# Kernel optimization log

Measured on AMD Instinct MI355X. Metric: run time of the kernel, lower is better.

The kernel has to match this reference:

```python
import jax, jax.numpy as jnp
import numpy as np

B, S = 10000, 32        # batch nodes, sampled neighbors per node
N, D_IN, D_H = 100000, 512, 512


def setup_inputs() -> dict:
    key = jax.random.key(0)
    k1, k2, k3 = jax.random.split(key, 3)
    neigh_idx = jax.random.randint(k1, (B, S), 0, N)                 # int neighbor ids
    features = jax.random.normal(k2, (N, D_IN), dtype=jnp.float32)   # node feature table
    W = jax.random.normal(k3, (D_H, D_IN), dtype=jnp.float32) * (1.0 / np.sqrt(D_IN))
    b = jnp.zeros((D_H,), dtype=jnp.float32)
    return {"neigh_idx": neigh_idx, "features": features, "W": W, "b": b}


def reference(neigh_idx, features, W, b):
    # gather neighbor embeddings: [B, S, D_IN]
    neigh_feats = features[neigh_idx]
    # MLP: Linear(input_dim, hidden_dim) + ReLU  -> [B, S, D_H]
    h = jax.nn.relu(jnp.einsum("bsd,hd->bsh", neigh_feats, W) + b)
    # mask-based mean pool over sampled neighbors (mask @ embed / row_sum) -> [B, D_H]
    return jnp.mean(h, axis=1)
```

## Files before the change

### kernel.cpp

```cpp
#include <hip/hip_runtime.h>
#include <hip/hip_bf16.h>


#define S_NB 32
#define D_IN 512
#define D_H  512
#define BM   128
#define BN   128
#define BK   64
#define NNODE 100000
#define NBATCH 10000
#define NTILE_N 4
#define NTILE_M 784
#define NTILES  (NTILE_N * NTILE_M)

typedef __attribute__((ext_vector_type(8))) short  short8;
typedef __attribute__((ext_vector_type(4))) float  f32x4;
typedef __attribute__((ext_vector_type(4))) unsigned short us4;
typedef __attribute__((ext_vector_type(8))) unsigned short us8;

__device__ __forceinline__ unsigned short f2bf(float x) {
  union { float f; unsigned u; } v; v.f = x;
  unsigned r = v.u + 0x7FFFu + ((v.u >> 16) & 1u);
  return (unsigned short)(r >> 16);
}

__device__ __forceinline__ float bf2f(unsigned short x) {
  union { unsigned u; float f; } v; v.u = ((unsigned)x) << 16;
  return v.f;
}

__device__ __forceinline__ int swz(int row, int cb) {
  return row * 128 + (cb ^ ((row & 7) << 4));
}

__device__ __forceinline__ void gld_lds16(const unsigned short* g, unsigned short* l) {
  __builtin_amdgcn_global_load_lds(
      (const __attribute__((address_space(1))) unsigned int*)g,
      (__attribute__((address_space(3))) unsigned int*)l, 16, 0, 0);
}

__global__ __launch_bounds__(256, 8)
void cvt_bf16(const float* __restrict__ src, unsigned short* __restrict__ dst, int n8) {
  int i = blockIdx.x * blockDim.x + threadIdx.x;
  const int stride = gridDim.x * blockDim.x;
  for (; i < n8; i += stride) {
    f32x4 a = *(const f32x4*)(src + (size_t)i * 8);
    f32x4 b = *(const f32x4*)(src + (size_t)i * 8 + 4);
    us8 o;
    o[0] = f2bf(a.x); o[1] = f2bf(a.y); o[2] = f2bf(a.z); o[3] = f2bf(a.w);
    o[4] = f2bf(b.x); o[5] = f2bf(b.y); o[6] = f2bf(b.z); o[7] = f2bf(b.w);
    *(us8*)(dst + (size_t)i * 8) = o;
  }
}

__global__ __launch_bounds__(256, 3)
void gemm_hf2(const float* __restrict__ feat,
              const unsigned short* __restrict__ Wb,
              const float* __restrict__ bias,
              unsigned short* __restrict__ Hb) {
  const int tid  = threadIdx.x;
  const int lane = tid & 63;
  const int wid  = tid >> 6;
  const int wr   = wid >> 1;
  const int wc   = wid & 1;

  const int bid  = blockIdx.x;
  const int tile = (bid & 7) * (NTILES / 8) + (bid >> 3);
  const int n0   = (tile & 3) * BN;
  const int m0   = (tile >> 2) * BM;

  __shared__ __align__(16) unsigned short As[BM * BK];
  __shared__ __align__(16) unsigned short Bs[2][BM * BK];

  const int lr = tid >> 4;
  const int lc = tid & 15;
  const float* aptr[8];
  int awoff[8];
#pragma unroll
  for (int p = 0; p < 8; ++p) {
    int row = p * 16 + lr;
    int gr  = m0 + row; if (gr > NNODE - 1) gr = NNODE - 1;
    aptr[p]  = feat + (size_t)gr * D_IN + lc * 4;
    awoff[p] = swz(row, lc * 8);
  }

  const unsigned short* srcW[4];
  int wdoff[4];
#pragma unroll
  for (int i = 0; i < 4; ++i) {
    int rl = wid * 32 + i * 8 + (lane >> 3);
    int g  = (lane & 7) ^ (rl & 7);
    srcW[i]  = Wb + (size_t)(n0 + rl) * D_IN + g * 8;
    wdoff[i] = (wid * 32 + i * 8) * 64;
  }

  f32x4 acc[4][4];
#pragma unroll
  for (int i = 0; i < 4; ++i)
#pragma unroll
    for (int j = 0; j < 4; ++j)
      acc[i][j] = (f32x4){0.f, 0.f, 0.f, 0.f};

  const int frow = lane & 15;
  const int kcb  = (lane >> 4) * 16;
  const int arow = wr * 64 + frow;
  const int brow = wc * 64 + frow;

  {
    f32x4 a0[8];
#pragma unroll
    for (int p = 0; p < 8; ++p) a0[p] = *(const f32x4*)(aptr[p]);
#pragma unroll
    for (int i = 0; i < 4; ++i) gld_lds16(srcW[i], &Bs[0][wdoff[i]]);
#pragma unroll
    for (int p = 0; p < 8; ++p) {
      us4 v;
      v.x = f2bf(a0[p].x); v.y = f2bf(a0[p].y); v.z = f2bf(a0[p].z); v.w = f2bf(a0[p].w);
      *(us4*)((char*)As + awoff[p]) = v;
    }
  }
  __syncthreads();

#pragma unroll
  for (int ki = 0; ki < D_IN / BK; ++ki) {
    const int cur = ki & 1;

    f32x4 an[8];
    if (ki < D_IN / BK - 1) {
#pragma unroll
      for (int p = 0; p < 8; ++p) an[p] = *(const f32x4*)(aptr[p] + (ki + 1) * BK);
#pragma unroll
      for (int i = 0; i < 4; ++i) gld_lds16(srcW[i] + (ki + 1) * BK, &Bs[cur ^ 1][wdoff[i]]);
    }

#pragma unroll
    for (int kk = 0; kk < 2; ++kk) {
      short8 af[4], bfr[4];
#pragma unroll
      for (int mi = 0; mi < 4; ++mi)
        af[mi] = *(const short8*)((const char*)As + swz(arow + mi * 16, kk * 64 + kcb));
#pragma unroll
      for (int ni = 0; ni < 4; ++ni)
        bfr[ni] = *(const short8*)((const char*)Bs[cur] + swz(brow + ni * 16, kk * 64 + kcb));
#pragma unroll
      for (int mi = 0; mi < 4; ++mi)
#pragma unroll
        for (int ni = 0; ni < 4; ++ni)
          acc[mi][ni] = __builtin_amdgcn_mfma_f32_16x16x32_bf16(af[mi], bfr[ni], acc[mi][ni], 0, 0, 0);
    }

    __syncthreads();

    if (ki < D_IN / BK - 1) {
#pragma unroll
      for (int p = 0; p < 8; ++p) {
        us4 v;
        v.x = f2bf(an[p].x); v.y = f2bf(an[p].y); v.z = f2bf(an[p].z); v.w = f2bf(an[p].w);
        *(us4*)((char*)As + awoff[p]) = v;
      }
    }
    __syncthreads();
  }

  unsigned short* Cs = &Bs[0][0];
  const int rq = lane >> 4;
#pragma unroll
  for (int ni = 0; ni < 4; ++ni) {
    int col = wc * 64 + ni * 16 + frow;
    float bv = bias[n0 + col];
#pragma unroll
    for (int mi = 0; mi < 4; ++mi) {
#pragma unroll
      for (int r = 0; r < 4; ++r) {
        int row = wr * 64 + mi * 16 + rq * 4 + r;
        int byt = row * 256 + ((col * 2) ^ ((row & 7) << 4));
        *(unsigned short*)((char*)Cs + byt) = f2bf(fmaxf(acc[mi][ni][r] + bv, 0.f));
      }
    }
  }
  __syncthreads();

  const int srow = tid >> 4;
  const int scol = (tid & 15) * 8;
#pragma unroll
  for (int it = 0; it < 8; ++it) {
    int row  = it * 16 + srow;
    int grow = m0 + row;
    int byt  = row * 256 + (((tid & 15) * 16) ^ ((row & 7) << 4));
    us8 v = *(const us8*)((const char*)Cs + byt);
    if (grow < NNODE)
      *(us8*)(Hb + (size_t)grow * D_H + n0 + scol) = v;
  }
}

__global__ __launch_bounds__(256, 8)
void pool_mean4(const unsigned short* __restrict__ Hb,
                const int* __restrict__ nidx,
                float* __restrict__ out) {
  const int b4 = blockIdx.x;
  const int q  = threadIdx.x >> 6;
  const int t  = threadIdx.x & 63;
  const int b  = b4 * 4 + q;

  __shared__ int rows[4][S_NB];
  if (threadIdx.x < 4 * S_NB)
    rows[threadIdx.x >> 5][threadIdx.x & 31] = nidx[b4 * 4 * S_NB + threadIdx.x];
  __syncthreads();

  const int c = t * 8;
  float s0 = 0.f, s1 = 0.f, s2 = 0.f, s3 = 0.f;
  float s4 = 0.f, s5 = 0.f, s6 = 0.f, s7 = 0.f;
#pragma unroll
  for (int s = 0; s < S_NB; ++s) {
    us8 v = *(const us8*)(Hb + (size_t)rows[q][s] * D_H + c);
    s0 += bf2f(v[0]); s1 += bf2f(v[1]); s2 += bf2f(v[2]); s3 += bf2f(v[3]);
    s4 += bf2f(v[4]); s5 += bf2f(v[5]); s6 += bf2f(v[6]); s7 += bf2f(v[7]);
  }
  const float inv = 1.0f / (float)S_NB;
  f32x4 o1; o1.x = s0 * inv; o1.y = s1 * inv; o1.z = s2 * inv; o1.w = s3 * inv;
  f32x4 o2; o2.x = s4 * inv; o2.y = s5 * inv; o2.z = s6 * inv; o2.w = s7 * inv;
  *(f32x4*)(out + (size_t)b * D_H + c)     = o1;
  *(f32x4*)(out + (size_t)b * D_H + c + 4) = o2;
}

__global__ __launch_bounds__(256, 4)
void gemm_h(const float* __restrict__ feat,
            const float* __restrict__ Wm,
            const float* __restrict__ bias,
            unsigned short* __restrict__ Hb) {
  const int tid  = threadIdx.x;
  const int lane = tid & 63;
  const int wid  = tid >> 6;
  const int wr   = wid >> 1;
  const int wc   = wid & 1;
  const int n0   = blockIdx.x * BN;
  const int m0   = blockIdx.y * BM;

  __shared__ __align__(16) unsigned short As[BM * BK];
  __shared__ __align__(16) unsigned short Bs[BM * BK];

  const int lr = tid >> 4;
  const int lc = tid & 15;

  const float* aptr[8];
  const float* wptr[8];
#pragma unroll
  for (int p = 0; p < 8; ++p) {
    int row = p * 16 + lr;
    int gr  = m0 + row; if (gr > NNODE - 1) gr = NNODE - 1;
    aptr[p] = feat + (size_t)gr * D_IN + lc * 4;
    wptr[p] = Wm + (size_t)(n0 + row) * D_IN + lc * 4;
  }

  f32x4 acc[4][4];
#pragma unroll
  for (int i = 0; i < 4; ++i)
#pragma unroll
    for (int j = 0; j < 4; ++j)
      acc[i][j] = (f32x4){0.f, 0.f, 0.f, 0.f};

  const int frow = lane & 15;
  const int kcb  = (lane >> 4) * 16;
  const int arow = wr * 64 + frow;
  const int brow = wc * 64 + frow;

  for (int k0 = 0; k0 < D_IN; k0 += BK) {
    __syncthreads();
#pragma unroll
    for (int p = 0; p < 8; ++p) {
      int row = p * 16 + lr;
      f32x4 av = *(const f32x4*)(aptr[p] + k0);
      f32x4 wv = *(const f32x4*)(wptr[p] + k0);
      us4 a4, w4;
      a4.x = f2bf(av.x); a4.y = f2bf(av.y); a4.z = f2bf(av.z); a4.w = f2bf(av.w);
      w4.x = f2bf(wv.x); w4.y = f2bf(wv.y); w4.z = f2bf(wv.z); w4.w = f2bf(wv.w);
      *(us4*)((char*)As + swz(row, lc * 8)) = a4;
      *(us4*)((char*)Bs + swz(row, lc * 8)) = w4;
    }
    __syncthreads();

#pragma unroll
    for (int kk = 0; kk < 2; ++kk) {
      short8 af[4], bfr[4];
#pragma unroll
      for (int mi = 0; mi < 4; ++mi)
        af[mi] = *(const short8*)((const char*)As + swz(arow + mi * 16, kk * 64 + kcb));
#pragma unroll
      for (int ni = 0; ni < 4; ++ni)
        bfr[ni] = *(const short8*)((const char*)Bs + swz(brow + ni * 16, kk * 64 + kcb));
#pragma unroll
      for (int mi = 0; mi < 4; ++mi)
#pragma unroll
        for (int ni = 0; ni < 4; ++ni)
          acc[mi][ni] = __builtin_amdgcn_mfma_f32_16x16x32_bf16(af[mi], bfr[ni], acc[mi][ni], 0, 0, 0);
    }
  }

  const int rq = lane >> 4;
#pragma unroll
  for (int ni = 0; ni < 4; ++ni) {
    int col = n0 + wc * 64 + ni * 16 + frow;
    float bv = bias[col];
#pragma unroll
    for (int mi = 0; mi < 4; ++mi) {
#pragma unroll
      for (int r = 0; r < 4; ++r) {
        int grow = m0 + wr * 64 + mi * 16 + rq * 4 + r;
        if (grow < NNODE)
          Hb[(size_t)grow * D_H + col] = f2bf(fmaxf(acc[mi][ni][r] + bv, 0.f));
      }
    }
  }
}

__global__ __launch_bounds__(256, 4)
void pool_aggr_gemm(const int* __restrict__ nidx_g,
                    const float* __restrict__ feat,
                    const float* __restrict__ Wm,
                    const float* __restrict__ bias,
                    float* __restrict__ out) {
  const int tid  = threadIdx.x;
  const int lane = tid & 63;
  const int wid  = tid >> 6;
  const int wr   = wid >> 1;
  const int wc   = wid & 1;
  const int n0   = blockIdx.x * BN;
  const int mb   = blockIdx.y;

  __shared__ __align__(16) unsigned short As[BM * BK];
  __shared__ __align__(16) unsigned short Bs[BM * BK];
  __shared__ int nid[BM];

  if (tid < BM) nid[tid] = nidx_g[mb * BM + tid];
  __syncthreads();

  const int lr = tid >> 4;
  const int lc = tid & 15;

  const float* aptr[8];
  const float* wptr[8];
#pragma unroll
  for (int p = 0; p < 8; ++p) {
    int row = p * 16 + lr;
    aptr[p] = feat + (size_t)nid[row] * D_IN + lc * 4;
    wptr[p] = Wm + (size_t)(n0 + row) * D_IN + lc * 4;
  }

  f32x4 acc[4][4];
#pragma unroll
  for (int i = 0; i < 4; ++i)
#pragma unroll
    for (int j = 0; j < 4; ++j)
      acc[i][j] = (f32x4){0.f, 0.f, 0.f, 0.f};

  const int frow = lane & 15;
  const int kcb  = (lane >> 4) * 16;
  const int arow = wr * 64 + frow;
  const int brow = wc * 64 + frow;

  for (int k0 = 0; k0 < D_IN; k0 += BK) {
    __syncthreads();
#pragma unroll
    for (int p = 0; p < 8; ++p) {
      int row = p * 16 + lr;
      f32x4 av = *(const f32x4*)(aptr[p] + k0);
      f32x4 wv = *(const f32x4*)(wptr[p] + k0);
      us4 a4, w4;
      a4.x = f2bf(av.x); a4.y = f2bf(av.y); a4.z = f2bf(av.z); a4.w = f2bf(av.w);
      w4.x = f2bf(wv.x); w4.y = f2bf(wv.y); w4.z = f2bf(wv.z); w4.w = f2bf(wv.w);
      *(us4*)((char*)As + swz(row, lc * 8)) = a4;
      *(us4*)((char*)Bs + swz(row, lc * 8)) = w4;
    }
    __syncthreads();

#pragma unroll
    for (int kk = 0; kk < 2; ++kk) {
      short8 af[4], bfr[4];
#pragma unroll
      for (int mi = 0; mi < 4; ++mi)
        af[mi] = *(const short8*)((const char*)As + swz(arow + mi * 16, kk * 64 + kcb));
#pragma unroll
      for (int ni = 0; ni < 4; ++ni)
        bfr[ni] = *(const short8*)((const char*)Bs + swz(brow + ni * 16, kk * 64 + kcb));
#pragma unroll
      for (int mi = 0; mi < 4; ++mi)
#pragma unroll
        for (int ni = 0; ni < 4; ++ni)
          acc[mi][ni] = __builtin_amdgcn_mfma_f32_16x16x32_bf16(af[mi], bfr[ni], acc[mi][ni], 0, 0, 0);
    }
  }

  const int rq = lane >> 4;
#pragma unroll
  for (int ni = 0; ni < 4; ++ni) {
    int col = n0 + wc * 64 + ni * 16 + frow;
    float bv = bias[col];
#pragma unroll
    for (int bl = 0; bl < 2; ++bl) {
      float s = 0.f;
#pragma unroll
      for (int m2 = 0; m2 < 2; ++m2) {
        int mi = bl * 2 + m2;
#pragma unroll
        for (int r = 0; r < 4; ++r)
          s += fmaxf(acc[mi][ni][r] + bv, 0.f);
      }
      s += __shfl_xor(s, 16);
      s += __shfl_xor(s, 32);
      if (rq == 0) {
        int bb = mb * 4 + wr * 2 + bl;
        out[(size_t)bb * D_H + col] = s * (1.0f / (float)S_NB);
      }
    }
  }
}

extern "C" void kernel_launch(void* const* d_in, const int* in_sizes, int n_in,
                              void* d_out, int out_size, void* d_ws, size_t ws_size,
                              hipStream_t stream) {
  const int*   nidx = (const int*)d_in[0];
  const float* feat = (const float*)d_in[1];
  const float* Wm   = (const float*)d_in[2];
  const float* bias = (const float*)d_in[3];
  float* out = (float*)d_out;

  const size_t wb_elems = (size_t)D_H * D_IN;
  const size_t wb_bytes = wb_elems * sizeof(unsigned short);
  const size_t h_bytes  = (size_t)NNODE * D_H * sizeof(unsigned short);

  if (ws_size >= wb_bytes + h_bytes) {
    unsigned short* Wb = (unsigned short*)d_ws;
    unsigned short* Hb = Wb + wb_elems;
    cvt_bf16<<<128, 256, 0, stream>>>(Wm, Wb, D_H * D_IN / 8);
    gemm_hf2<<<NTILES, 256, 0, stream>>>(feat, Wb, bias, Hb);
    pool_mean4<<<NBATCH / 4, 256, 0, stream>>>(Hb, nidx, out);
  } else if (ws_size >= h_bytes) {
    unsigned short* Hb = (unsigned short*)d_ws;
    dim3 g1(D_H / BN, (NNODE + BM - 1) / BM);
    gemm_h<<<g1, 256, 0, stream>>>(feat, Wm, bias, Hb);
    pool_mean4<<<NBATCH / 4, 256, 0, stream>>>(Hb, nidx, out);
  } else {
    dim3 grid(D_H / BN, NBATCH / 4);
    pool_aggr_gemm<<<grid, 256, 0, stream>>>(nidx, feat, Wm, bias, out);
  }
}
```

Measured before the change: 204.4 us.

## Deepen GEMM prefetch pipeline with manual waitcnt and raw barriers

The fp32 feature loads for the A tile are now issued two K-steps ahead instead of one, with W tiles still async-copied into double-buffered LDS. Full __syncthreads are replaced by explicit s_waitcnt vmcnt/lgkmcnt plus s_barrier and sched_barrier hints, so the waits block only on the data needed now. This is meant to hide global-memory latency behind the MFMA work. The vmcnt(12) count is hand-tuned and must match the number of outstanding loads exactly, or the kernel reads stale data.

```diff
diff --git a/kernel.cpp b/kernel.cpp
--- a/kernel.cpp
+++ b/kernel.cpp
@@ -8,6 +8,7 @@
 #define BM   128
 #define BN   128
 #define BK   64
+#define NK   (D_IN / BK)
 #define NNODE 100000
 #define NBATCH 10000
 #define NTILE_N 4
@@ -18,6 +19,12 @@
 typedef __attribute__((ext_vector_type(4))) float  f32x4;
 typedef __attribute__((ext_vector_type(4))) unsigned short us4;
 typedef __attribute__((ext_vector_type(8))) unsigned short us8;
+
+#define WAITVM12() asm volatile("s_waitcnt vmcnt(12)" ::: "memory")
+#define WAITVM0()  asm volatile("s_waitcnt vmcnt(0)" ::: "memory")
+#define WAITLGKM0() asm volatile("s_waitcnt lgkmcnt(0)" ::: "memory")
+#define SBAR()   __builtin_amdgcn_s_barrier()
+#define SCHED0() __builtin_amdgcn_sched_barrier(0)
 
 __device__ __forceinline__ unsigned short f2bf(float x) {
   union { float f; unsigned u; } v; v.f = x;
@@ -55,7 +62,7 @@
 }
 
 __global__ __launch_bounds__(256, 3)
-void gemm_hf2(const float* __restrict__ feat,
+void gemm_hf3(const float* __restrict__ feat,
               const unsigned short* __restrict__ Wb,
               const float* __restrict__ bias,
               unsigned short* __restrict__ Hb) {
@@ -107,32 +114,37 @@
   const int arow = wr * 64 + frow;
   const int brow = wc * 64 + frow;
 
+  f32x4 aN[8];
   {
+#pragma unroll
+    for (int i = 0; i < 4; ++i) gld_lds16(srcW[i], &Bs[0][wdoff[i]]);
     f32x4 a0[8];
 #pragma unroll
     for (int p = 0; p < 8; ++p) a0[p] = *(const f32x4*)(aptr[p]);
-#pragma unroll
-    for (int i = 0; i < 4; ++i) gld_lds16(srcW[i], &Bs[0][wdoff[i]]);
 #pragma unroll
     for (int p = 0; p < 8; ++p) {
       us4 v;
       v.x = f2bf(a0[p].x); v.y = f2bf(a0[p].y); v.z = f2bf(a0[p].z); v.w = f2bf(a0[p].w);
       *(us4*)((char*)As + awoff[p]) = v;
     }
-  }
-  __syncthreads();
-
-#pragma unroll
-  for (int ki = 0; ki < D_IN / BK; ++ki) {
+#pragma unroll
+    for (int p = 0; p < 8; ++p) aN[p] = *(const f32x4*)(aptr[p] + BK);
+    SCHED0();
+  }
+
+#pragma unroll
+  for (int ki = 0; ki < NK; ++ki) {
     const int cur = ki & 1;
 
-    f32x4 an[8];
-    if (ki < D_IN / BK - 1) {
-#pragma unroll
-      for (int p = 0; p < 8; ++p) an[p] = *(const f32x4*)(aptr[p] + (ki + 1) * BK);
+    if (ki < NK - 1) {
 #pragma unroll
       for (int i = 0; i < 4; ++i) gld_lds16(srcW[i] + (ki + 1) * BK, &Bs[cur ^ 1][wdoff[i]]);
     }
+
+    if (ki < NK - 1) { WAITVM12(); } else { WAITVM0(); }
+    WAITLGKM0();
+    SBAR();
+    SCHED0();
 
 #pragma unroll
     for (int kk = 0; kk < 2; ++kk) {
@@ -150,17 +162,22 @@
           acc[mi][ni] = __builtin_amdgcn_mfma_f32_16x16x32_bf16(af[mi], bfr[ni], acc[mi][ni], 0, 0, 0);
     }
 
-    __syncthreads();
-
-    if (ki < D_IN / BK - 1) {
+    SBAR();
+    SCHED0();
+
+    if (ki < NK - 1) {
 #pragma unroll
       for (int p = 0; p < 8; ++p) {
         us4 v;
-        v.x = f2bf(an[p].x); v.y = f2bf(an[p].y); v.z = f2bf(an[p].z); v.w = f2bf(an[p].w);
+        v.x = f2bf(aN[p].x); v.y = f2bf(aN[p].y); v.z = f2bf(aN[p].z); v.w = f2bf(aN[p].w);
         *(us4*)((char*)As + awoff[p]) = v;
       }
-    }
-    __syncthreads();
+      if (ki < NK - 2) {
+#pragma unroll
+        for (int p = 0; p < 8; ++p) aN[p] = *(const f32x4*)(aptr[p] + (ki + 2) * BK);
+        SCHED0();
+      }
+    }
   }
 
   unsigned short* Cs = &Bs[0][0];
@@ -433,7 +450,7 @@
     unsigned short* Wb = (unsigned short*)d_ws;
     unsigned short* Hb = Wb + wb_elems;
     cvt_bf16<<<128, 256, 0, stream>>>(Wm, Wb, D_H * D_IN / 8);
-    gemm_hf2<<<NTILES, 256, 0, stream>>>(feat, Wb, bias, Hb);
+    gemm_hf3<<<NTILES, 256, 0, stream>>>(feat, Wb, bias, Hb);
     pool_mean4<<<NBATCH / 4, 256, 0, stream>>>(Hb, nidx, out);
   } else if (ws_size >= h_bytes) {
     unsigned short* Hb = (unsigned short*)d_ws;
```

Result: slower. 234.3 us (+14.6%).

## Stream fp32 features directly to LDS via async loads, convert to bf16 at fragment read

Applied to the files above, without the earlier changes.

The main GEMM now loads fp32 feature tiles straight into double-buffered LDS with global_load_lds instead of staging through registers and converting before the LDS store. Conversion to bf16 moves to fragment-read time using packed bf16x2 conversion intrinsics. BK is halved to 32 so the fp32 tiles fit in LDS, which drops one of the two barriers per k-step and adds a new XOR swizzle for both A and W tiles. The cost is twice as many k-iterations, redundant conversions (each A element is converted by both column waves), and LDS read traffic doubled for A.

```diff
diff --git a/kernel.cpp b/kernel.cpp
--- a/kernel.cpp
+++ b/kernel.cpp
@@ -7,7 +7,8 @@
 #define D_H  512
 #define BM   128
 #define BN   128
-#define BK   64
+#define BK   32
+#define NK   (D_IN / BK)
 #define NNODE 100000
 #define NBATCH 10000
 #define NTILE_N 4
@@ -30,11 +31,22 @@
   return v.f;
 }
 
+__device__ __forceinline__ short8 cvt8bf(f32x4 lo, f32x4 hi) {
+  union { __hip_bfloat162 h; unsigned u; } c0, c1, c2, c3;
+  c0.h = __float22bfloat162_rn(make_float2(lo.x, lo.y));
+  c1.h = __float22bfloat162_rn(make_float2(lo.z, lo.w));
+  c2.h = __float22bfloat162_rn(make_float2(hi.x, hi.y));
+  c3.h = __float22bfloat162_rn(make_float2(hi.z, hi.w));
+  union { unsigned u[4]; short8 s; } r;
+  r.u[0] = c0.u; r.u[1] = c1.u; r.u[2] = c2.u; r.u[3] = c3.u;
+  return r.s;
+}
+
 __device__ __forceinline__ int swz(int row, int cb) {
   return row * 128 + (cb ^ ((row & 7) << 4));
 }
 
-__device__ __forceinline__ void gld_lds16(const unsigned short* g, unsigned short* l) {
+__device__ __forceinline__ void gld_lds16(const void* g, void* l) {
   __builtin_amdgcn_global_load_lds(
       (const __attribute__((address_space(1))) unsigned int*)g,
       (__attribute__((address_space(3))) unsigned int*)l, 16, 0, 0);
@@ -55,10 +67,10 @@
 }
 
 __global__ __launch_bounds__(256, 3)
-void gemm_hf2(const float* __restrict__ feat,
-              const unsigned short* __restrict__ Wb,
-              const float* __restrict__ bias,
-              unsigned short* __restrict__ Hb) {
+void gemm_f32a(const float* __restrict__ feat,
+               const unsigned short* __restrict__ Wb,
+               const float* __restrict__ bias,
+               unsigned short* __restrict__ Hb) {
   const int tid  = threadIdx.x;
   const int lane = tid & 63;
   const int wid  = tid >> 6;
@@ -70,29 +82,31 @@
   const int n0   = (tile & 3) * BN;
   const int m0   = (tile >> 2) * BM;
 
-  __shared__ __align__(16) unsigned short As[BM * BK];
-  __shared__ __align__(16) unsigned short Bs[2][BM * BK];
-
-  const int lr = tid >> 4;
-  const int lc = tid & 15;
-  const float* aptr[8];
-  int awoff[8];
-#pragma unroll
-  for (int p = 0; p < 8; ++p) {
-    int row = p * 16 + lr;
+  __shared__ __align__(16) float          As[2][BM * BK];
+  __shared__ __align__(16) unsigned short Ws[2][64 * 64];
+
+  const float* srcA[4];
+  int dstAoff[4];
+#pragma unroll
+  for (int i = 0; i < 4; ++i) {
+    int row = wid * 32 + i * 8 + (lane >> 3);
+    int p   = lane & 7;
     int gr  = m0 + row; if (gr > NNODE - 1) gr = NNODE - 1;
-    aptr[p]  = feat + (size_t)gr * D_IN + lc * 4;
-    awoff[p] = swz(row, lc * 8);
-  }
-
-  const unsigned short* srcW[4];
-  int wdoff[4];
-#pragma unroll
-  for (int i = 0; i < 4; ++i) {
-    int rl = wid * 32 + i * 8 + (lane >> 3);
-    int g  = (lane & 7) ^ (rl & 7);
-    srcW[i]  = Wb + (size_t)(n0 + rl) * D_IN + g * 8;
-    wdoff[i] = (wid * 32 + i * 8) * 64;
+    srcA[i]   = feat + (size_t)gr * D_IN + (p ^ (row & 7)) * 4;
+    dstAoff[i] = (wid * 32 + i * 8) * BK;
+  }
+
+  const unsigned short* srcW[2];
+  int dstWoff[2];
+#pragma unroll
+  for (int i = 0; i < 2; ++i) {
+    int c = wid * 2 + i;
+    int L = c * 8 + (lane >> 3);
+    int p = lane & 7;
+    int q = p ^ (L & 7);
+    int rowbit = q >> 2, g0 = q & 3;
+    srcW[i]   = Wb + (size_t)(n0 + L * 2 + rowbit) * D_IN + g0 * 8;
+    dstWoff[i] = c * 512;
   }
 
   f32x4 acc[4][4];
@@ -103,67 +117,55 @@
       acc[i][j] = (f32x4){0.f, 0.f, 0.f, 0.f};
 
   const int frow = lane & 15;
-  const int kcb  = (lane >> 4) * 16;
+  const int jg   = lane >> 4;
   const int arow = wr * 64 + frow;
-  const int brow = wc * 64 + frow;
-
-  {
-    f32x4 a0[8];
-#pragma unroll
-    for (int p = 0; p < 8; ++p) a0[p] = *(const f32x4*)(aptr[p]);
-#pragma unroll
-    for (int i = 0; i < 4; ++i) gld_lds16(srcW[i], &Bs[0][wdoff[i]]);
-#pragma unroll
-    for (int p = 0; p < 8; ++p) {
-      us4 v;
-      v.x = f2bf(a0[p].x); v.y = f2bf(a0[p].y); v.z = f2bf(a0[p].z); v.w = f2bf(a0[p].w);
-      *(us4*)((char*)As + awoff[p]) = v;
-    }
-  }
+  const int ag1 = ((2 * jg) ^ (frow & 7)) * 16;
+  const int ag2 = ((2 * jg + 1) ^ (frow & 7)) * 16;
+  const int wp  = ((((frow & 1) << 2) + jg) ^ ((frow >> 1) & 7)) * 16;
+  const int wlb = wc * 32 + (frow >> 1);
+
+#pragma unroll
+  for (int i = 0; i < 4; ++i) gld_lds16(srcA[i], &As[0][dstAoff[i]]);
+#pragma unroll
+  for (int i = 0; i < 2; ++i) gld_lds16(srcW[i], &Ws[0][dstWoff[i]]);
   __syncthreads();
 
 #pragma unroll
-  for (int ki = 0; ki < D_IN / BK; ++ki) {
+  for (int ki = 0; ki < NK; ++ki) {
     const int cur = ki & 1;
 
-    f32x4 an[8];
-    if (ki < D_IN / BK - 1) {
-#pragma unroll
-      for (int p = 0; p < 8; ++p) an[p] = *(const f32x4*)(aptr[p] + (ki + 1) * BK);
-#pragma unroll
-      for (int i = 0; i < 4; ++i) gld_lds16(srcW[i] + (ki + 1) * BK, &Bs[cur ^ 1][wdoff[i]]);
-    }
-
-#pragma unroll
-    for (int kk = 0; kk < 2; ++kk) {
-      short8 af[4], bfr[4];
-#pragma unroll
-      for (int mi = 0; mi < 4; ++mi)
-        af[mi] = *(const short8*)((const char*)As + swz(arow + mi * 16, kk * 64 + kcb));
+    if (ki < NK - 1) {
+#pragma unroll
+      for (int i = 0; i < 4; ++i)
+        gld_lds16(srcA[i] + (ki + 1) * BK, &As[cur ^ 1][dstAoff[i]]);
+#pragma unroll
+      for (int i = 0; i < 2; ++i)
+        gld_lds16(srcW[i] + (ki + 1) * BK, &Ws[cur ^ 1][dstWoff[i]]);
+    }
+
+    short8 af[4], bfr[4];
+#pragma unroll
+    for (int mi = 0; mi < 4; ++mi) {
+      const char* base = (const char*)&As[cur][0] + (arow + mi * 16) * 128;
+      f32x4 lo = *(const f32x4*)(base + ag1);
+      f32x4 hi = *(const f32x4*)(base + ag2);
+      af[mi] = cvt8bf(lo, hi);
+    }
+#pragma unroll
+    for (int ni = 0; ni < 4; ++ni) {
+      const char* base = (const char*)&Ws[cur][0] + (wlb + ni * 8) * 128;
+      bfr[ni] = *(const short8*)(base + wp);
+    }
+#pragma unroll
+    for (int mi = 0; mi < 4; ++mi)
 #pragma unroll
       for (int ni = 0; ni < 4; ++ni)
-        bfr[ni] = *(const short8*)((const char*)Bs[cur] + swz(brow + ni * 16, kk * 64 + kcb));
-#pragma unroll
-      for (int mi = 0; mi < 4; ++mi)
-#pragma unroll
-        for (int ni = 0; ni < 4; ++ni)
-          acc[mi][ni] = __builtin_amdgcn_mfma_f32_16x16x32_bf16(af[mi], bfr[ni], acc[mi][ni], 0, 0, 0);
-    }
+        acc[mi][ni] = __builtin_amdgcn_mfma_f32_16x16x32_bf16(af[mi], bfr[ni], acc[mi][ni], 0, 0, 0);
 
     __syncthreads();
-
-    if (ki < D_IN / BK - 1) {
-#pragma unroll
-      for (int p = 0; p < 8; ++p) {
-        us4 v;
-        v.x = f2bf(an[p].x); v.y = f2bf(an[p].y); v.z = f2bf(an[p].z); v.w = f2bf(an[p].w);
-        *(us4*)((char*)As + awoff[p]) = v;
-      }
-    }
-    __syncthreads();
-  }
-
-  unsigned short* Cs = &Bs[0][0];
+  }
+
+  unsigned short* Cs = (unsigned short*)&As[0][0];
   const int rq = lane >> 4;
 #pragma unroll
   for (int ni = 0; ni < 4; ++ni) {
@@ -237,8 +239,8 @@
   const int n0   = blockIdx.x * BN;
   const int m0   = blockIdx.y * BM;
 
-  __shared__ __align__(16) unsigned short As[BM * BK];
-  __shared__ __align__(16) unsigned short Bs[BM * BK];
+  __shared__ __align__(16) unsigned short As[BM * 64];
+  __shared__ __align__(16) unsigned short Bs[BM * 64];
 
   const int lr = tid >> 4;
   const int lc = tid & 15;
@@ -265,7 +267,7 @@
   const int arow = wr * 64 + frow;
   const int brow = wc * 64 + frow;
 
-  for (int k0 = 0; k0 < D_IN; k0 += BK) {
+  for (int k0 = 0; k0 < D_IN; k0 += 64) {
     __syncthreads();
 #pragma unroll
     for (int p = 0; p < 8; ++p) {
@@ -328,8 +330,8 @@
   const int n0   = blockIdx.x * BN;
   const int mb   = blockIdx.y;
 
-  __shared__ __align__(16) unsigned short As[BM * BK];
-  __shared__ __align__(16) unsigned short Bs[BM * BK];
+  __shared__ __align__(16) unsigned short As[BM * 64];
+  __shared__ __align__(16) unsigned short Bs[BM * 64];
   __shared__ int nid[BM];
 
   if (tid < BM) nid[tid] = nidx_g[mb * BM + tid];
@@ -359,7 +361,7 @@
   const int arow = wr * 64 + frow;
   const int brow = wc * 64 + frow;
 
-  for (int k0 = 0; k0 < D_IN; k0 += BK) {
+  for (int k0 = 0; k0 < D_IN; k0 += 64) {
     __syncthreads();
 #pragma unroll
     for (int p = 0; p < 8; ++p) {
@@ -433,7 +435,7 @@
     unsigned short* Wb = (unsigned short*)d_ws;
     unsigned short* Hb = Wb + wb_elems;
     cvt_bf16<<<128, 256, 0, stream>>>(Wm, Wb, D_H * D_IN / 8);
-    gemm_hf2<<<NTILES, 256, 0, stream>>>(feat, Wb, bias, Hb);
+    gemm_f32a<<<NTILES, 256, 0, stream>>>(feat, Wb, bias, Hb);
     pool_mean4<<<NBATCH / 4, 256, 0, stream>>>(Hb, nidx, out);
   } else if (ws_size >= h_bytes) {
     unsigned short* Hb = (unsigned short*)d_ws;
```

Result: faster. 191.8 us (-6.1%).
